# Kernel tuning notes

Measured on AMD Instinct MI355X. Metric: run time of the kernel, lower is better.

The kernel has to match this reference:

```python
import jax, jax.numpy as jnp
import numpy as np

B, S, D = 4, 2048, 1024   # batch, seq, in_dim
E, K, H = 8, 2, 4096      # num_experts, top_k, expert hidden


def setup_inputs() -> dict:
    key = jax.random.key(0)
    ks = jax.random.split(key, 10)
    s = lambda *sh: 1.0 / np.sqrt(sh[0])
    x = jax.random.normal(ks[0], (B, S, D), dtype=jnp.float32)
    # router: Linear(D,D) + GELU + Linear(D,E), xavier-ish init, zero bias
    Wr1 = jax.random.uniform(ks[1], (D, D), jnp.float32, -s(D), s(D))
    br1 = jnp.zeros((D,), jnp.float32)
    Wr2 = jax.random.uniform(ks[2], (D, E), jnp.float32, -s(D), s(D))
    br2 = jnp.zeros((E,), jnp.float32)
    # experts: stacked 2-layer MLPs, Linear(D,H)+GELU+Linear(H,D)
    W1 = jax.random.uniform(ks[3], (E, D, H), jnp.float32, -s(D), s(D))
    b1 = jnp.zeros((E, H), jnp.float32)
    W2 = jax.random.uniform(ks[4], (E, H, D), jnp.float32, -s(H), s(H))
    b2 = jnp.zeros((E, D), jnp.float32)
    return {"x": x, "Wr1": Wr1, "br1": br1, "Wr2": Wr2, "br2": br2,
            "W1": W1, "b1": b1, "W2": W2, "b2": b2}


def reference(x, Wr1, br1, Wr2, br2, W1, b1, W2, b2):
    T = B * S
    xf = x.reshape(T, D)                                   # [T, D]
    # router MLP -> softmax
    h = jax.nn.gelu(xf @ Wr1 + br1, approximate=False)
    logits = h @ Wr2 + br2                                 # [T, E]
    probs = jax.nn.softmax(logits, axis=-1)
    # top-k selection; scatter selected probs back into a sparse [T, E] map
    top_v, top_i = jax.lax.top_k(probs, K)                 # [T, K]
    rows = jnp.arange(T)[:, None]
    router_probs = jnp.zeros_like(probs).at[rows, top_i].set(top_v)
    # normalize=True, top_k>1: renormalize (gradient flows through sum)
    router_probs = router_probs / router_probs.sum(-1, keepdims=True)
    # combine: sum_e router_probs[:, e] * expert_e(x)
    # (router_probs is exactly zero for non-selected experts, matching the
    #  masked gather/scatter-add in the torch module)
    out = jnp.zeros_like(xf)
    for e in range(E):  # fixed small expert loop
        y = jax.nn.gelu(xf @ W1[e] + b1[e], approximate=False) @ W2[e] + b2[e]
        out = out + router_probs[:, e:e + 1] * y
    return out.reshape(B, S, D)
```

## Files before the change

kernel.cpp:

```cpp
#include <hip/hip_runtime.h>
#include <hip/hip_bf16.h>
#include <math.h>

#define T_TOK 8192
#define DIM   1024
#define NEXP  8
#define TOPK  2
#define HID   4096
#define NSLOT (T_TOK * TOPK)
#define FLAG_GAP 1e-4f
#define MAXFLAG  2048
#define MBLK     136

typedef unsigned short u16;
typedef __bf16 bf16x8 __attribute__((ext_vector_type(8)));
typedef float  f32x4  __attribute__((ext_vector_type(4)));
typedef u16    u16x4  __attribute__((ext_vector_type(4)));

#define GLL16(g, l) \
  __builtin_amdgcn_global_load_lds((__attribute__((address_space(1))) unsigned int*)(g), \
                                   (__attribute__((address_space(3))) unsigned int*)(l), 16, 0, 0)

__device__ __forceinline__ float bf2f(u16 u) {
  union { unsigned int i; float f; } w; w.i = ((unsigned int)u) << 16; return w.f;
}
__device__ __forceinline__ u16 f2bf(float f) {
  union { float f; unsigned int i; } w; w.f = f;
  unsigned int i = w.i;
  return (u16)((i + 0x7FFFu + ((i >> 16) & 1u)) >> 16);
}
__device__ __forceinline__ float gelu_f(float v) {
  return 0.5f * v * (1.0f + erff(v * 0.70710678118654752f));
}

__global__ __launch_bounds__(256) void split_cast(
    const float* __restrict__ in, u16* __restrict__ hi, u16* __restrict__ lo, int n4)
{
  int i = blockIdx.x * 256 + threadIdx.x;
  if (i >= n4) return;
  f32x4 v = *(const f32x4*)&in[(size_t)i * 4];
  u16x4 h, l;
#pragma unroll
  for (int j = 0; j < 4; j++) {
    h[j] = f2bf(v[j]);
    l[j] = f2bf(v[j] - bf2f(h[j]));
  }
  *(u16x4*)&hi[(size_t)i * 4] = h;
  *(u16x4*)&lo[(size_t)i * 4] = l;
}

__global__ __launch_bounds__(256) void transpose_cast(
    const float* __restrict__ in, u16* __restrict__ out, int R, int C)
{
  __shared__ u16 ld[64][65];
  const size_t mat = (size_t)R * C;
  const float* I = in + (size_t)blockIdx.z * mat;
  u16* O = out + (size_t)blockIdx.z * mat;
  const int c0 = blockIdx.x * 64, r0 = blockIdx.y * 64;
  const int tx = threadIdx.x & 15, ty = threadIdx.x >> 4;
#pragma unroll
  for (int p = 0; p < 4; p++) {
    int r = ty + p * 16;
    f32x4 v = *(const f32x4*)&I[(size_t)(r0 + r) * C + c0 + tx * 4];
    ld[r][tx * 4 + 0] = f2bf(v.x); ld[r][tx * 4 + 1] = f2bf(v.y);
    ld[r][tx * 4 + 2] = f2bf(v.z); ld[r][tx * 4 + 3] = f2bf(v.w);
  }
  __syncthreads();
#pragma unroll
  for (int p = 0; p < 4; p++) {
    int c = ty + p * 16;
    u16x4 v;
    v.x = ld[tx * 4 + 0][c]; v.y = ld[tx * 4 + 1][c];
    v.z = ld[tx * 4 + 2][c]; v.w = ld[tx * 4 + 3][c];
    *(u16x4*)&O[(size_t)(c0 + c) * R + r0 + tx * 4] = v;
  }
}

__global__ __launch_bounds__(256) void transpose_cast_split(
    const float* __restrict__ in, u16* __restrict__ Ohi, u16* __restrict__ Olo,
    int R, int C)
{
  __shared__ float ld[64][65];
  const int c0 = blockIdx.x * 64, r0 = blockIdx.y * 64;
  const int tx = threadIdx.x & 15, ty = threadIdx.x >> 4;
#pragma unroll
  for (int p = 0; p < 4; p++) {
    int r = ty + p * 16;
    f32x4 v = *(const f32x4*)&in[(size_t)(r0 + r) * C + c0 + tx * 4];
    ld[r][tx * 4 + 0] = v.x; ld[r][tx * 4 + 1] = v.y;
    ld[r][tx * 4 + 2] = v.z; ld[r][tx * 4 + 3] = v.w;
  }
  __syncthreads();
#pragma unroll
  for (int p = 0; p < 4; p++) {
    int c = ty + p * 16;
    u16x4 h, l;
#pragma unroll
    for (int j = 0; j < 4; j++) {
      float v = ld[tx * 4 + j][c];
      h[j] = f2bf(v);
      l[j] = f2bf(v - bf2f(h[j]));
    }
    *(u16x4*)&Ohi[(size_t)(c0 + c) * R + r0 + tx * 4] = h;
    *(u16x4*)&Olo[(size_t)(c0 + c) * R + r0 + tx * 4] = l;
  }
}

__global__ __launch_bounds__(256) void gemm1_split(
    const u16* __restrict__ Ahi, const u16* __restrict__ Alo,
    const u16* __restrict__ Bhi, const u16* __restrict__ Blo,
    const float* __restrict__ bias, float* __restrict__ Cout)
{
  const int r0 = blockIdx.y * 128, n0 = blockIdx.x * 128;
  __shared__ __align__(16) u16 Ah[128 * 32], Al[128 * 32];
  __shared__ __align__(16) u16 Bh[128 * 32], Bl[128 * 32];

  const int tid = threadIdx.x;
  const int wave = tid >> 6, lane = tid & 63;
  const int srow = lane >> 2, scol = (lane & 3) * 8;

  const u16 *aph[2], *apl[2], *bph[2], *bpl[2];
  u16 *ahd[2], *ald[2], *bhd[2], *bld[2];
#pragma unroll
  for (int i = 0; i < 2; i++) {
    int r = wave * 32 + i * 16 + srow;
    size_t arow = (size_t)(r0 + r) * DIM + scol;
    size_t brow = (size_t)(n0 + r) * DIM + scol;
    aph[i] = Ahi + arow; apl[i] = Alo + arow;
    bph[i] = Bhi + brow; bpl[i] = Blo + brow;
    ahd[i] = &Ah[(wave * 32 + i * 16) * 32]; ald[i] = &Al[(wave * 32 + i * 16) * 32];
    bhd[i] = &Bh[(wave * 32 + i * 16) * 32]; bld[i] = &Bl[(wave * 32 + i * 16) * 32];
  }

  f32x4 zero = {0.f, 0.f, 0.f, 0.f};
  f32x4 acc[4][4];
#pragma unroll
  for (int a = 0; a < 4; a++)
#pragma unroll
    for (int b = 0; b < 4; b++) acc[a][b] = zero;

  const int quad = lane >> 4, l16 = lane & 15;
  const int wm = (wave & 1) * 64, wn = (wave >> 1) * 64;

  for (int k0 = 0; k0 < DIM; k0 += 32) {
#pragma unroll
    for (int i = 0; i < 2; i++) {
      GLL16(aph[i] + k0, ahd[i]);
      GLL16(apl[i] + k0, ald[i]);
      GLL16(bph[i] + k0, bhd[i]);
      GLL16(bpl[i] + k0, bld[i]);
    }
    __syncthreads();
    bf16x8 ah[4], al[4], bh[4], bl[4];
#pragma unroll
    for (int mt = 0; mt < 4; mt++) {
      int ro = (wm + mt * 16 + l16) * 32 + quad * 8;
      ah[mt] = *(const bf16x8*)&Ah[ro];
      al[mt] = *(const bf16x8*)&Al[ro];
    }
#pragma unroll
    for (int nt = 0; nt < 4; nt++) {
      int ro = (wn + nt * 16 + l16) * 32 + quad * 8;
      bh[nt] = *(const bf16x8*)&Bh[ro];
      bl[nt] = *(const bf16x8*)&Bl[ro];
    }
#pragma unroll
    for (int mt = 0; mt < 4; mt++)
#pragma unroll
      for (int nt = 0; nt < 4; nt++) {
        acc[mt][nt] = __builtin_amdgcn_mfma_f32_16x16x32_bf16(ah[mt], bh[nt], acc[mt][nt], 0, 0, 0);
        acc[mt][nt] = __builtin_amdgcn_mfma_f32_16x16x32_bf16(ah[mt], bl[nt], acc[mt][nt], 0, 0, 0);
        acc[mt][nt] = __builtin_amdgcn_mfma_f32_16x16x32_bf16(al[mt], bh[nt], acc[mt][nt], 0, 0, 0);
      }
    __syncthreads();
  }

  float bv[4];
#pragma unroll
  for (int nt = 0; nt < 4; nt++) bv[nt] = bias[n0 + wn + nt * 16 + l16];

#pragma unroll
  for (int mt = 0; mt < 4; mt++)
#pragma unroll
    for (int reg = 0; reg < 4; reg++) {
      int r = wm + mt * 16 + quad * 4 + reg;
      size_t crow = (size_t)(r0 + r) * DIM;
#pragma unroll
      for (int nt = 0; nt < 4; nt++) {
        int c = n0 + wn + nt * 16 + l16;
        Cout[crow + c] = gelu_f(acc[mt][nt][reg] + bv[nt]);
      }
    }
}

template<int EPI, bool GATHER>
__global__ __launch_bounds__(256) void gemm_bt(
    const u16* __restrict__ A, const u16* __restrict__ BT,
    const float* __restrict__ bias,
    const int* __restrict__ counts, const int* __restrict__ offs,
    const int* __restrict__ map_e, const int* __restrict__ map_r0,
    const int* __restrict__ tok,
    u16* __restrict__ Cout, int N, int K)
{
  const int mb = blockIdx.y;
  const int e  = map_e[mb];
  if (e < 0) return;
  const int cnt  = counts[e];
  const int r0   = map_r0[mb];
  const int base = offs[e];
  const int n0   = blockIdx.x * 128;
  const u16* BTe = BT + (size_t)e * N * K;
  const float* be = bias + (size_t)e * N;

  __shared__ __align__(16) u16 As[128 * 32];
  __shared__ __align__(16) u16 Bs[128 * 32];

  const int tid = threadIdx.x;
  const int wave = tid >> 6, lane = tid & 63;
  const int srow = lane >> 2, scol = (lane & 3) * 8;

  const u16* ap[2]; const u16* bp[2];
  u16* asd[2]; u16* bsd[2];
#pragma unroll
  for (int i = 0; i < 2; i++) {
    int r  = wave * 32 + i * 16 + srow;
    int rr = min(r0 + r, cnt - 1);
    int arow = GATHER ? tok[base + rr] : (base + rr);
    ap[i] = A + (size_t)arow * K + scol;
    int nr = n0 + wave * 32 + i * 16 + srow;
    bp[i] = BTe + (size_t)nr * K + scol;
    asd[i] = &As[(wave * 32 + i * 16) * 32];
    bsd[i] = &Bs[(wave * 32 + i * 16) * 32];
  }

  f32x4 zero = {0.f, 0.f, 0.f, 0.f};
  f32x4 acc[4][4];
#pragma unroll
  for (int a = 0; a < 4; a++)
#pragma unroll
    for (int b = 0; b < 4; b++) acc[a][b] = zero;

  const int quad = lane >> 4, l16 = lane & 15;
  const int wm = (wave & 1) * 64, wn = (wave >> 1) * 64;

  for (int k0 = 0; k0 < K; k0 += 32) {
#pragma unroll
    for (int i = 0; i < 2; i++) {
      GLL16(ap[i] + k0, asd[i]);
      GLL16(bp[i] + k0, bsd[i]);
    }
    __syncthreads();
    bf16x8 af[4], bfv[4];
#pragma unroll
    for (int mt = 0; mt < 4; mt++)
      af[mt] = *(const bf16x8*)&As[(wm + mt * 16 + l16) * 32 + quad * 8];
#pragma unroll
    for (int nt = 0; nt < 4; nt++)
      bfv[nt] = *(const bf16x8*)&Bs[(wn + nt * 16 + l16) * 32 + quad * 8];
#pragma unroll
    for (int mt = 0; mt < 4; mt++)
#pragma unroll
      for (int nt = 0; nt < 4; nt++)
        acc[mt][nt] = __builtin_amdgcn_mfma_f32_16x16x32_bf16(
            af[mt], bfv[nt], acc[mt][nt], 0, 0, 0);
    __syncthreads();
  }

  float bv[4];
#pragma unroll
  for (int nt = 0; nt < 4; nt++) bv[nt] = be[n0 + wn + nt * 16 + l16];

#pragma unroll
  for (int mt = 0; mt < 4; mt++)
#pragma unroll
    for (int reg = 0; reg < 4; reg++) {
      int r = wm + mt * 16 + quad * 4 + reg;
      if (r0 + r < cnt) {
        size_t crow = (size_t)(base + r0 + r) * N;
#pragma unroll
        for (int nt = 0; nt < 4; nt++) {
          int c = n0 + wn + nt * 16 + l16;
          float v = acc[mt][nt][reg] + bv[nt];
          Cout[crow + c] = f2bf(EPI == 0 ? gelu_f(v) : v);
        }
      }
    }
}

__global__ __launch_bounds__(256) void router2a(
    const float* __restrict__ hr, const float* __restrict__ Wr2,
    const float* __restrict__ br2,
    float* __restrict__ logits, int* __restrict__ nflag, int* __restrict__ flaglist)
{
  __shared__ float w[NEXP * DIM];
  __shared__ float bsh[NEXP];
  const int tid = threadIdx.x;
  for (int i = tid; i < NEXP * DIM; i += 256) {
    int d = i >> 3, e2 = i & 7;
    w[e2 * DIM + d] = Wr2[i];
  }
  if (tid < NEXP) bsh[tid] = br2[tid];
  __syncthreads();
  const int wave = tid >> 6, lane = tid & 63;
  for (int tt = 0; tt < 4; tt++) {
    int t = blockIdx.x * 16 + wave * 4 + tt;
    float acc[NEXP] = {0, 0, 0, 0, 0, 0, 0, 0};
    for (int jj = 0; jj < 16; jj++) {
      int d = jj * 64 + lane;
      float hv = hr[(size_t)t * DIM + d];
#pragma unroll
      for (int e2 = 0; e2 < NEXP; e2++) acc[e2] += hv * w[e2 * DIM + d];
    }
#pragma unroll
    for (int off = 32; off > 0; off >>= 1)
#pragma unroll
      for (int e2 = 0; e2 < NEXP; e2++) acc[e2] += __shfl_xor(acc[e2], off, 64);
    if (lane == 0) {
      float l[NEXP];
#pragma unroll
      for (int e2 = 0; e2 < NEXP; e2++) {
        l[e2] = acc[e2] + bsh[e2];
        logits[(size_t)t * NEXP + e2] = l[e2];
      }
      int e0 = 0;
#pragma unroll
      for (int e2 = 1; e2 < NEXP; e2++) if (l[e2] > l[e0]) e0 = e2;
      int e1 = (e0 == 0) ? 1 : 0;
#pragma unroll
      for (int e2 = 0; e2 < NEXP; e2++) if (e2 != e0 && l[e2] > l[e1]) e1 = e2;
      float third = -1e30f;
#pragma unroll
      for (int e2 = 0; e2 < NEXP; e2++)
        if (e2 != e0 && e2 != e1 && l[e2] > third) third = l[e2];
      if (l[e1] - third < FLAG_GAP) {
        int idx = atomicAdd(nflag, 1);
        if (idx < MAXFLAG) flaglist[idx] = t;
      }
    }
  }
}

__global__ __launch_bounds__(256) void fixup_fp64(
    const float* __restrict__ x, const float* __restrict__ Wr1,
    const float* __restrict__ br1, const float* __restrict__ Wr2,
    const float* __restrict__ br2,
    const int* __restrict__ nflag, const int* __restrict__ flaglist,
    float* __restrict__ logits)
{
  int nf = *nflag; if (nf > MAXFLAG) nf = MAXFLAG;
  if ((int)blockIdx.x >= nf) return;
  const int t = flaglist[blockIdx.x];
  __shared__ float xs[DIM];
  __shared__ double part[256][NEXP];
  const int tid = threadIdx.x;
  for (int i = tid; i < DIM; i += 256) xs[i] = x[(size_t)t * DIM + i];
  __syncthreads();
  double h[4] = {0.0, 0.0, 0.0, 0.0};
  const int d0 = tid * 4;
  for (int k = 0; k < DIM; k++) {
    double xv = (double)xs[k];
    f32x4 wv = *(const f32x4*)&Wr1[(size_t)k * DIM + d0];
#pragma unroll
    for (int j = 0; j < 4; j++) h[j] = fma(xv, (double)wv[j], h[j]);
  }
  double lacc[NEXP] = {0, 0, 0, 0, 0, 0, 0, 0};
#pragma unroll
  for (int j = 0; j < 4; j++) {
    double v = h[j] + (double)br1[d0 + j];
    v = 0.5 * v * (1.0 + erf(v * 0.70710678118654752440));
#pragma unroll
    for (int e2 = 0; e2 < NEXP; e2++)
      lacc[e2] = fma(v, (double)Wr2[(size_t)(d0 + j) * NEXP + e2], lacc[e2]);
  }
#pragma unroll
  for (int e2 = 0; e2 < NEXP; e2++) part[tid][e2] = lacc[e2];
  __syncthreads();
  if (tid < NEXP) {
    double s = (double)br2[tid];
    for (int i = 0; i < 256; i++) s += part[i][tid];
    logits[(size_t)t * NEXP + tid] = (float)s;
  }
}

__global__ __launch_bounds__(256) void finalize_route(
    const float* __restrict__ logits, float2* __restrict__ gates,
    int* __restrict__ experts, int* __restrict__ counts)
{
  __shared__ int lc[NEXP];
  const int tid = threadIdx.x;
  if (tid < NEXP) lc[tid] = 0;
  __syncthreads();
  const int t = blockIdx.x * 256 + tid;
  float l[NEXP];
#pragma unroll
  for (int e2 = 0; e2 < NEXP; e2++) l[e2] = logits[(size_t)t * NEXP + e2];
  int e0 = 0;
#pragma unroll
  for (int e2 = 1; e2 < NEXP; e2++) if (l[e2] > l[e0]) e0 = e2;
  int e1 = (e0 == 0) ? 1 : 0;
#pragma unroll
  for (int e2 = 0; e2 < NEXP; e2++) if (e2 != e0 && l[e2] > l[e1]) e1 = e2;
  float p1 = expf(l[e1] - l[e0]);
  float s = 1.0f + p1;
  gates[t] = make_float2(1.0f / s, p1 / s);
  experts[2 * t]     = e0;
  experts[2 * t + 1] = e1;
  atomicAdd(&lc[e0], 1); atomicAdd(&lc[e1], 1);
  __syncthreads();
  if (tid < NEXP && lc[tid]) atomicAdd(&counts[tid], lc[tid]);
}

__global__ void zero_meta(int* meta) {
  if (threadIdx.x < 32) meta[threadIdx.x] = 0;
}

__global__ void prefix8(const int* __restrict__ counts, int* __restrict__ offs,
                        int* __restrict__ cursor,
                        int* __restrict__ map_e, int* __restrict__ map_r0) {
  if (threadIdx.x == 0) {
    int a = 0, m = 0;
    for (int e = 0; e < NEXP; e++) {
      offs[e] = a; cursor[e] = a;
      int nb = (counts[e] + 127) >> 7;
      for (int j = 0; j < nb; j++) { map_e[m] = e; map_r0[m] = j << 7; m++; }
      a += counts[e];
    }
    for (; m < MBLK; m++) { map_e[m] = -1; map_r0[m] = 0; }
  }
}

__global__ __launch_bounds__(256) void scatter_tok(
    const int* __restrict__ experts, int* __restrict__ cursor,
    int* __restrict__ tok_of_slot, int* __restrict__ slot_of_token)
{
  int idx = blockIdx.x * 256 + threadIdx.x;
  int e = experts[idx];
  int slot = atomicAdd(&cursor[e], 1);
  tok_of_slot[slot] = idx >> 1;
  slot_of_token[idx] = slot;
}

__global__ __launch_bounds__(256) void combine(
    const u16* __restrict__ y, const float2* __restrict__ gates,
    const int* __restrict__ slot_of_token, float* __restrict__ out)
{
  int t = blockIdx.x, tid = threadIdx.x;
  int s0 = slot_of_token[2 * t], s1 = slot_of_token[2 * t + 1];
  float2 g = gates[t];
  u16x4 a = *(const u16x4*)&y[(size_t)s0 * DIM + tid * 4];
  u16x4 b = *(const u16x4*)&y[(size_t)s1 * DIM + tid * 4];
  f32x4 o;
#pragma unroll
  for (int j = 0; j < 4; j++) o[j] = g.x * bf2f(a[j]) + g.y * bf2f(b[j]);
  *(f32x4*)&out[(size_t)t * DIM + tid * 4] = o;
}

extern "C" void kernel_launch(void* const* d_in, const int* in_sizes, int n_in,
                              void* d_out, int out_size, void* d_ws, size_t ws_size,
                              hipStream_t stream)
{
  const float* x   = (const float*)d_in[0];
  const float* Wr1 = (const float*)d_in[1];
  const float* br1 = (const float*)d_in[2];
  const float* Wr2 = (const float*)d_in[3];
  const float* br2 = (const float*)d_in[4];
  const float* W1  = (const float*)d_in[5];
  const float* b1  = (const float*)d_in[6];
  const float* W2  = (const float*)d_in[7];
  const float* b2  = (const float*)d_in[8];
  float* out = (float*)d_out;

  char* ws = (char*)d_ws;
  const size_t MB = 1024 * 1024;
  u16*   xhi    = (u16*)  (ws + 0 * MB);
  u16*   xlo    = (u16*)  (ws + 16 * MB);
  u16*   Wr1Thi = (u16*)  (ws + 32 * MB);
  u16*   Wr1Tlo = (u16*)  (ws + 34 * MB);
  u16*   W1T    = (u16*)  (ws + 36 * MB);
  u16*   W2T    = (u16*)  (ws + 100 * MB);
  u16*   hidden = (u16*)  (ws + 164 * MB);
  float* hr32   = (float*)(ws + 164 * MB);
  u16*   y      = (u16*)  (ws + 0 * MB);
  char* tail = ws + 292 * MB;
  float*  logits = (float*)tail;                      tail += (size_t)T_TOK * NEXP * 4;
  float2* gates  = (float2*)tail;                     tail += (size_t)T_TOK * 8;
  int* experts       = (int*)tail;                    tail += (size_t)NSLOT * 4;
  int* tok_of_slot   = (int*)tail;                    tail += (size_t)NSLOT * 4;
  int* slot_of_token = (int*)tail;                    tail += (size_t)NSLOT * 4;
  int* flaglist      = (int*)tail;                    tail += (size_t)MAXFLAG * 4;
  int* map_e         = (int*)tail;                    tail += (size_t)MBLK * 4;
  int* map_r0        = (int*)tail;                    tail += (size_t)MBLK * 4;
  int* meta          = (int*)tail;
  int* counts = meta, *offs = meta + 8, *cursor = meta + 16, *nflag = meta + 24;

  zero_meta<<<1, 64, 0, stream>>>(meta);
  split_cast<<<T_TOK * DIM / 1024, 256, 0, stream>>>(x, xhi, xlo, T_TOK * DIM / 4);
  transpose_cast_split<<<dim3(16, 16, 1), 256, 0, stream>>>(Wr1, Wr1Thi, Wr1Tlo, DIM, DIM);
  transpose_cast<<<dim3(64, 16, NEXP), 256, 0, stream>>>(W1, W1T, DIM, HID);
  transpose_cast<<<dim3(16, 64, NEXP), 256, 0, stream>>>(W2, W2T, HID, DIM);
  gemm1_split<<<dim3(DIM / 128, T_TOK / 128), 256, 0, stream>>>(
      xhi, xlo, Wr1Thi, Wr1Tlo, br1, hr32);
  router2a<<<T_TOK / 16, 256, 0, stream>>>(hr32, Wr2, br2, logits, nflag, flaglist);
  fixup_fp64<<<MAXFLAG, 256, 0, stream>>>(x, Wr1, br1, Wr2, br2, nflag, flaglist, logits);
  finalize_route<<<T_TOK / 256, 256, 0, stream>>>(logits, gates, experts, counts);
  prefix8<<<1, 64, 0, stream>>>(counts, offs, cursor, map_e, map_r0);
  scatter_tok<<<NSLOT / 256, 256, 0, stream>>>(experts, cursor,
                                               tok_of_slot, slot_of_token);
  gemm_bt<0, true><<<dim3(HID / 128, MBLK), 256, 0, stream>>>(
      xhi, W1T, b1, counts, offs, map_e, map_r0, tok_of_slot, hidden, HID, DIM);
  gemm_bt<1, false><<<dim3(DIM / 128, MBLK), 256, 0, stream>>>(
      hidden, W2T, b2, counts, offs, map_e, map_r0, nullptr, y, DIM, HID);
  combine<<<T_TOK, 256, 0, stream>>>(y, gates, slot_of_token, out);
}
```

Before: 1.190 ms.

## Swizzle LDS tiles, deepen expert GEMM K-step, shrink router tile, fast GELU

Several unrelated changes land together. The expert GEMMs now load 64-wide K tiles into LDS with an XOR-style rotated column layout, which halves the barrier count and cuts bank conflicts. The router GEMM uses 128x64 tiles with the same swizzle, launching more blocks for better occupancy. Exact erff in GELU is swapped for an Abramowitz-Stegun polynomial with a fast exp and reciprocal, which risks small accuracy loss. The fp64 fixup kernel splits the K reduction across waves so its Wr1 reads coalesce better.

Result: faster. 987.5 us (-17.0%).

```diff
diff --git a/kernel.cpp b/kernel.cpp
--- a/kernel.cpp
+++ b/kernel.cpp
@@ -29,8 +29,17 @@
   unsigned int i = w.i;
   return (u16)((i + 0x7FFFu + ((i >> 16) & 1u)) >> 16);
 }
-__device__ __forceinline__ float gelu_f(float v) {
-  return 0.5f * v * (1.0f + erff(v * 0.70710678118654752f));
+__device__ __forceinline__ float erf_fast(float x) {
+  float ax = fabsf(x);
+  float t = __builtin_amdgcn_rcpf(1.0f + 0.3275911f * ax);
+  float p = t * (0.254829592f + t * (-0.284496736f + t * (1.421413741f +
+            t * (-1.453152027f + t * 1.061405429f))));
+  float e = __expf(-ax * ax);
+  float r = 1.0f - p * e;
+  return x < 0.0f ? -r : r;
+}
+__device__ __forceinline__ float gelu_fast(float v) {
+  return 0.5f * v * (1.0f + erf_fast(v * 0.70710678118654752f));
 }
 
 __global__ __launch_bounds__(256) void split_cast(
@@ -111,63 +120,70 @@
     const u16* __restrict__ Bhi, const u16* __restrict__ Blo,
     const float* __restrict__ bias, float* __restrict__ Cout)
 {
-  const int r0 = blockIdx.y * 128, n0 = blockIdx.x * 128;
+  const int r0 = blockIdx.y * 128, n0 = blockIdx.x * 64;
   __shared__ __align__(16) u16 Ah[128 * 32], Al[128 * 32];
-  __shared__ __align__(16) u16 Bh[128 * 32], Bl[128 * 32];
+  __shared__ __align__(16) u16 Bh[64 * 32],  Bl[64 * 32];
 
   const int tid = threadIdx.x;
   const int wave = tid >> 6, lane = tid & 63;
-  const int srow = lane >> 2, scol = (lane & 3) * 8;
-
-  const u16 *aph[2], *apl[2], *bph[2], *bpl[2];
-  u16 *ahd[2], *ald[2], *bhd[2], *bld[2];
-#pragma unroll
-  for (int i = 0; i < 2; i++) {
-    int r = wave * 32 + i * 16 + srow;
-    size_t arow = (size_t)(r0 + r) * DIM + scol;
-    size_t brow = (size_t)(n0 + r) * DIM + scol;
-    aph[i] = Ahi + arow; apl[i] = Alo + arow;
-    bph[i] = Bhi + brow; bpl[i] = Blo + brow;
-    ahd[i] = &Ah[(wave * 32 + i * 16) * 32]; ald[i] = &Al[(wave * 32 + i * 16) * 32];
-    bhd[i] = &Bh[(wave * 32 + i * 16) * 32]; bld[i] = &Bl[(wave * 32 + i * 16) * 32];
-  }
+  const int srow = lane >> 2;
+  const int slot = lane & 3;
+
+  const u16 *ahp[2], *alp[2]; u16 *ahd[2], *aldd[2];
+#pragma unroll
+  for (int s = 0; s < 2; s++) {
+    int row = wave * 32 + s * 16 + srow;
+    int c = (slot - row) & 3;
+    size_t g = (size_t)(r0 + row) * DIM + c * 8;
+    ahp[s] = Ahi + g; alp[s] = Alo + g;
+    ahd[s] = &Ah[(wave * 32 + s * 16) * 32];
+    aldd[s] = &Al[(wave * 32 + s * 16) * 32];
+  }
+  int brow = wave * 16 + srow;
+  int cb = (slot - brow) & 3;
+  const u16* bhp = Bhi + (size_t)(n0 + brow) * DIM + cb * 8;
+  const u16* blp = Blo + (size_t)(n0 + brow) * DIM + cb * 8;
+  u16* bhd = &Bh[(wave * 16) * 32];
+  u16* bld = &Bl[(wave * 16) * 32];
 
   f32x4 zero = {0.f, 0.f, 0.f, 0.f};
-  f32x4 acc[4][4];
+  f32x4 acc[4][2];
 #pragma unroll
   for (int a = 0; a < 4; a++)
 #pragma unroll
-    for (int b = 0; b < 4; b++) acc[a][b] = zero;
+    for (int b = 0; b < 2; b++) acc[a][b] = zero;
 
   const int quad = lane >> 4, l16 = lane & 15;
-  const int wm = (wave & 1) * 64, wn = (wave >> 1) * 64;
+  const int wm = (wave & 1) * 64, wn = (wave >> 1) * 32;
 
   for (int k0 = 0; k0 < DIM; k0 += 32) {
 #pragma unroll
-    for (int i = 0; i < 2; i++) {
-      GLL16(aph[i] + k0, ahd[i]);
-      GLL16(apl[i] + k0, ald[i]);
-      GLL16(bph[i] + k0, bhd[i]);
-      GLL16(bpl[i] + k0, bld[i]);
-    }
+    for (int s = 0; s < 2; s++) {
+      GLL16(ahp[s] + k0, ahd[s]);
+      GLL16(alp[s] + k0, aldd[s]);
+    }
+    GLL16(bhp + k0, bhd);
+    GLL16(blp + k0, bld);
     __syncthreads();
-    bf16x8 ah[4], al[4], bh[4], bl[4];
+    bf16x8 ah[4], al[4], bh[2], bl[2];
 #pragma unroll
     for (int mt = 0; mt < 4; mt++) {
-      int ro = (wm + mt * 16 + l16) * 32 + quad * 8;
-      ah[mt] = *(const bf16x8*)&Ah[ro];
-      al[mt] = *(const bf16x8*)&Al[ro];
-    }
-#pragma unroll
-    for (int nt = 0; nt < 4; nt++) {
-      int ro = (wn + nt * 16 + l16) * 32 + quad * 8;
-      bh[nt] = *(const bf16x8*)&Bh[ro];
-      bl[nt] = *(const bf16x8*)&Bl[ro];
+      int R = wm + mt * 16 + l16;
+      int off = R * 32 + ((quad + R) & 3) * 8;
+      ah[mt] = *(const bf16x8*)&Ah[off];
+      al[mt] = *(const bf16x8*)&Al[off];
+    }
+#pragma unroll
+    for (int nt = 0; nt < 2; nt++) {
+      int R = wn + nt * 16 + l16;
+      int off = R * 32 + ((quad + R) & 3) * 8;
+      bh[nt] = *(const bf16x8*)&Bh[off];
+      bl[nt] = *(const bf16x8*)&Bl[off];
     }
 #pragma unroll
     for (int mt = 0; mt < 4; mt++)
 #pragma unroll
-      for (int nt = 0; nt < 4; nt++) {
+      for (int nt = 0; nt < 2; nt++) {
         acc[mt][nt] = __builtin_amdgcn_mfma_f32_16x16x32_bf16(ah[mt], bh[nt], acc[mt][nt], 0, 0, 0);
         acc[mt][nt] = __builtin_amdgcn_mfma_f32_16x16x32_bf16(ah[mt], bl[nt], acc[mt][nt], 0, 0, 0);
         acc[mt][nt] = __builtin_amdgcn_mfma_f32_16x16x32_bf16(al[mt], bh[nt], acc[mt][nt], 0, 0, 0);
@@ -175,9 +191,9 @@
     __syncthreads();
   }
 
-  float bv[4];
-#pragma unroll
-  for (int nt = 0; nt < 4; nt++) bv[nt] = bias[n0 + wn + nt * 16 + l16];
+  float bv[2];
+#pragma unroll
+  for (int nt = 0; nt < 2; nt++) bv[nt] = bias[n0 + wn + nt * 16 + l16];
 
 #pragma unroll
   for (int mt = 0; mt < 4; mt++)
@@ -186,9 +202,9 @@
       int r = wm + mt * 16 + quad * 4 + reg;
       size_t crow = (size_t)(r0 + r) * DIM;
 #pragma unroll
-      for (int nt = 0; nt < 4; nt++) {
+      for (int nt = 0; nt < 2; nt++) {
         int c = n0 + wn + nt * 16 + l16;
-        Cout[crow + c] = gelu_f(acc[mt][nt][reg] + bv[nt]);
+        Cout[crow + c] = gelu_fast(acc[mt][nt][reg] + bv[nt]);
       }
     }
 }
@@ -212,25 +228,27 @@
   const u16* BTe = BT + (size_t)e * N * K;
   const float* be = bias + (size_t)e * N;
 
-  __shared__ __align__(16) u16 As[128 * 32];
-  __shared__ __align__(16) u16 Bs[128 * 32];
+  __shared__ __align__(16) u16 As[128 * 64];
+  __shared__ __align__(16) u16 Bs[128 * 64];
 
   const int tid = threadIdx.x;
   const int wave = tid >> 6, lane = tid & 63;
-  const int srow = lane >> 2, scol = (lane & 3) * 8;
-
-  const u16* ap[2]; const u16* bp[2];
-  u16* asd[2]; u16* bsd[2];
-#pragma unroll
-  for (int i = 0; i < 2; i++) {
-    int r  = wave * 32 + i * 16 + srow;
-    int rr = min(r0 + r, cnt - 1);
+  const int srow = lane >> 3;
+  const int slot = lane & 7;
+
+  const u16 *agp[4], *bgp[4];
+  u16 *ald[4], *bld[4];
+#pragma unroll
+  for (int s = 0; s < 4; s++) {
+    int row = wave * 32 + s * 8 + srow;
+    int c = (slot - row) & 7;
+    int rr = min(r0 + row, cnt - 1);
     int arow = GATHER ? tok[base + rr] : (base + rr);
-    ap[i] = A + (size_t)arow * K + scol;
-    int nr = n0 + wave * 32 + i * 16 + srow;
-    bp[i] = BTe + (size_t)nr * K + scol;
-    asd[i] = &As[(wave * 32 + i * 16) * 32];
-    bsd[i] = &Bs[(wave * 32 + i * 16) * 32];
+    agp[s] = A + (size_t)arow * K + c * 8;
+    ald[s] = &As[(wave * 32 + s * 8) * 64];
+    int nr = n0 + row;
+    bgp[s] = BTe + (size_t)nr * K + c * 8;
+    bld[s] = &Bs[(wave * 32 + s * 8) * 64];
   }
 
   f32x4 zero = {0.f, 0.f, 0.f, 0.f};
@@ -243,26 +261,33 @@
   const int quad = lane >> 4, l16 = lane & 15;
   const int wm = (wave & 1) * 64, wn = (wave >> 1) * 64;
 
-  for (int k0 = 0; k0 < K; k0 += 32) {
-#pragma unroll
-    for (int i = 0; i < 2; i++) {
-      GLL16(ap[i] + k0, asd[i]);
-      GLL16(bp[i] + k0, bsd[i]);
+  for (int k0 = 0; k0 < K; k0 += 64) {
+#pragma unroll
+    for (int s = 0; s < 4; s++) {
+      GLL16(agp[s] + k0, ald[s]);
+      GLL16(bgp[s] + k0, bld[s]);
     }
     __syncthreads();
-    bf16x8 af[4], bfv[4];
-#pragma unroll
-    for (int mt = 0; mt < 4; mt++)
-      af[mt] = *(const bf16x8*)&As[(wm + mt * 16 + l16) * 32 + quad * 8];
-#pragma unroll
-    for (int nt = 0; nt < 4; nt++)
-      bfv[nt] = *(const bf16x8*)&Bs[(wn + nt * 16 + l16) * 32 + quad * 8];
-#pragma unroll
-    for (int mt = 0; mt < 4; mt++)
-#pragma unroll
-      for (int nt = 0; nt < 4; nt++)
-        acc[mt][nt] = __builtin_amdgcn_mfma_f32_16x16x32_bf16(
-            af[mt], bfv[nt], acc[mt][nt], 0, 0, 0);
+#pragma unroll
+    for (int kk = 0; kk < 2; kk++) {
+      bf16x8 af[4], bfv[4];
+#pragma unroll
+      for (int mt = 0; mt < 4; mt++) {
+        int R = wm + mt * 16 + l16;
+        af[mt] = *(const bf16x8*)&As[R * 64 + ((kk * 4 + quad + R) & 7) * 8];
+      }
+#pragma unroll
+      for (int nt = 0; nt < 4; nt++) {
+        int R = wn + nt * 16 + l16;
+        bfv[nt] = *(const bf16x8*)&Bs[R * 64 + ((kk * 4 + quad + R) & 7) * 8];
+      }
+#pragma unroll
+      for (int mt = 0; mt < 4; mt++)
+#pragma unroll
+        for (int nt = 0; nt < 4; nt++)
+          acc[mt][nt] = __builtin_amdgcn_mfma_f32_16x16x32_bf16(
+              af[mt], bfv[nt], acc[mt][nt], 0, 0, 0);
+    }
     __syncthreads();
   }
 
@@ -281,7 +306,7 @@
         for (int nt = 0; nt < 4; nt++) {
           int c = n0 + wn + nt * 16 + l16;
           float v = acc[mt][nt][reg] + bv[nt];
-          Cout[crow + c] = f2bf(EPI == 0 ? gelu_f(v) : v);
+          Cout[crow + c] = f2bf(EPI == 0 ? gelu_fast(v) : v);
         }
       }
     }
@@ -351,33 +376,44 @@
   if ((int)blockIdx.x >= nf) return;
   const int t = flaglist[blockIdx.x];
   __shared__ float xs[DIM];
-  __shared__ double part[256][NEXP];
-  const int tid = threadIdx.x;
+  __shared__ double hpart[4][DIM];
+  const int tid = threadIdx.x, wave = tid >> 6, lane = tid & 63;
   for (int i = tid; i < DIM; i += 256) xs[i] = x[(size_t)t * DIM + i];
   __syncthreads();
-  double h[4] = {0.0, 0.0, 0.0, 0.0};
-  const int d0 = tid * 4;
-  for (int k = 0; k < DIM; k++) {
+  double h[4][4] = {};
+  for (int ki = 0; ki < 256; ki++) {
+    int k = wave * 256 + ki;
     double xv = (double)xs[k];
-    f32x4 wv = *(const f32x4*)&Wr1[(size_t)k * DIM + d0];
-#pragma unroll
-    for (int j = 0; j < 4; j++) h[j] = fma(xv, (double)wv[j], h[j]);
-  }
+#pragma unroll
+    for (int g = 0; g < 4; g++) {
+      f32x4 wv = *(const f32x4*)&Wr1[(size_t)k * DIM + g * 256 + lane * 4];
+#pragma unroll
+      for (int j = 0; j < 4; j++) h[g][j] = fma(xv, (double)wv[j], h[g][j]);
+    }
+  }
+#pragma unroll
+  for (int g = 0; g < 4; g++)
+#pragma unroll
+    for (int j = 0; j < 4; j++) hpart[wave][g * 256 + lane * 4 + j] = h[g][j];
+  __syncthreads();
   double lacc[NEXP] = {0, 0, 0, 0, 0, 0, 0, 0};
 #pragma unroll
   for (int j = 0; j < 4; j++) {
-    double v = h[j] + (double)br1[d0 + j];
+    int d = tid * 4 + j;
+    double v = hpart[0][d] + hpart[1][d] + hpart[2][d] + hpart[3][d] + (double)br1[d];
     v = 0.5 * v * (1.0 + erf(v * 0.70710678118654752440));
 #pragma unroll
     for (int e2 = 0; e2 < NEXP; e2++)
-      lacc[e2] = fma(v, (double)Wr2[(size_t)(d0 + j) * NEXP + e2], lacc[e2]);
-  }
-#pragma unroll
-  for (int e2 = 0; e2 < NEXP; e2++) part[tid][e2] = lacc[e2];
+      lacc[e2] = fma(v, (double)Wr2[(size_t)d * NEXP + e2], lacc[e2]);
+  }
+  __syncthreads();
+  double* red = &hpart[0][0];
+#pragma unroll
+  for (int e2 = 0; e2 < NEXP; e2++) red[tid * NEXP + e2] = lacc[e2];
   __syncthreads();
   if (tid < NEXP) {
     double s = (double)br2[tid];
-    for (int i = 0; i < 256; i++) s += part[i][tid];
+    for (int i = 0; i < 256; i++) s += red[i * NEXP + tid];
     logits[(size_t)t * NEXP + tid] = (float)s;
   }
 }
@@ -498,7 +534,7 @@
   transpose_cast_split<<<dim3(16, 16, 1), 256, 0, stream>>>(Wr1, Wr1Thi, Wr1Tlo, DIM, DIM);
   transpose_cast<<<dim3(64, 16, NEXP), 256, 0, stream>>>(W1, W1T, DIM, HID);
   transpose_cast<<<dim3(16, 64, NEXP), 256, 0, stream>>>(W2, W2T, HID, DIM);
-  gemm1_split<<<dim3(DIM / 128, T_TOK / 128), 256, 0, stream>>>(
+  gemm1_split<<<dim3(DIM / 64, T_TOK / 128), 256, 0, stream>>>(
       xhi, xlo, Wr1Thi, Wr1Tlo, br1, hr32);
   router2a<<<T_TOK / 16, 256, 0, stream>>>(hr32, Wr2, br2, logits, nflag, flaglist);
   fixup_fp64<<<MAXFLAG, 256, 0, stream>>>(x, Wr1, br1, Wr2, br2, nflag, flaglist, logits);
```
